# Performance work log

Hardware: AMD Instinct MI355X
Metric: run time of the kernel (lower is better)

The kernel has to match this reference:

```python
import jax, jax.numpy as jnp
import numpy as np

B, S, M, E, H = 4, 2048, 1024, 8, 4096
CAP = 2 * (B * S) // E  # GShard top-2 capacity = 2*s/e = 2048


def setup_inputs() -> dict:
    key = jax.random.key(0)
    k = jax.random.split(key, 6)
    sc = 0.02
    return {
        "x": jax.random.normal(k[0], (B, S, M), jnp.float32),
        "wg": jax.random.normal(k[1], (M, E), jnp.float32) * sc,
        "w1": jax.random.normal(k[2], (E, M, H), jnp.float32) * sc,
        "b1": jnp.zeros((E, H), jnp.float32),
        "w2": jax.random.normal(k[3], (E, H, M), jnp.float32) * sc,
        "b2": jnp.zeros((E, M), jnp.float32),
    }


def top2gating(logits, capacity):
    # Faithful GShard/fairscale top2gating: logits [s, e]
    s, e = logits.shape
    gates = jax.nn.softmax(logits, axis=-1)
    idx1 = jnp.argmax(gates, axis=1)
    mask1 = jax.nn.one_hot(idx1, e, dtype=jnp.float32)
    logits2 = jnp.where(mask1 > 0, -jnp.inf, logits)
    idx2 = jnp.argmax(logits2, axis=1)
    mask2 = jax.nn.one_hot(idx2, e, dtype=jnp.float32)
    # positions within each expert's buffer
    loc1 = jnp.cumsum(mask1, axis=0) - 1.0
    loc2 = jnp.cumsum(mask2, axis=0) - 1.0 + jnp.sum(mask1, axis=0, keepdims=True)
    # load-balancing aux loss (computed before capacity drop, per fairscale)
    me = jnp.mean(gates, axis=0)
    ce = jnp.mean(mask1, axis=0)
    l_aux = jnp.mean(me * ce) * (e * e)
    # drop tokens over capacity
    mask1 = mask1 * (loc1 < capacity)
    mask2 = mask2 * (loc2 < capacity)
    loc1_s = jnp.sum(loc1 * mask1, axis=1).astype(jnp.int32)
    loc2_s = jnp.sum(loc2 * mask2, axis=1).astype(jnp.int32)
    gates1 = jnp.sum(gates * mask1, axis=1)
    gates2 = jnp.sum(gates * mask2, axis=1)
    denom = jnp.maximum(gates1 + gates2, 1e-9)
    gates1 = gates1 / denom
    gates2 = gates2 / denom
    # dense [s, e, c] combine weights (as in the original einsum formulation)
    oh1 = jax.nn.one_hot(loc1_s, capacity, dtype=jnp.float32)
    oh2 = jax.nn.one_hot(loc2_s, capacity, dtype=jnp.float32)
    combine = (gates1[:, None] * mask1)[:, :, None] * oh1[:, None, :] \
            + (gates2[:, None] * mask2)[:, :, None] * oh2[:, None, :]
    dispatch = combine > 0
    return l_aux, combine, dispatch


def reference(x, wg, w1, b1, w2, b2):
    d_model = x.shape[2]
    xf = x.reshape(-1, d_model)                      # [s, m]
    logits = xf @ wg                                 # [s, e]
    l_aux, combine, dispatch = top2gating(logits, CAP)
    # dispatch: dense one-hot scatter, as in torch.einsum('sec,sm->ecm')
    disp = jnp.einsum('sec,sm->ecm', dispatch.astype(xf.dtype), xf)
    # per-expert FFN (Linear -> ReLU -> Linear), vectorized over experts
    h = jax.nn.relu(jnp.einsum('ecm,emh->ech', disp, w1) + b1[:, None, :])
    eo = jnp.einsum('ech,ehm->ecm', h, w2) + b2[:, None, :]
    # combine: torch.einsum('sec,ecm->sm')
    out = jnp.einsum('sec,ecm->sm', combine, eo)
    return out.reshape(x.shape), l_aux
```

## Files before the change

kernel.cpp:

```cpp
#include <hip/hip_runtime.h>
#include <stdint.h>

typedef unsigned short u16;
typedef __attribute__((ext_vector_type(8))) short bf16x8;
typedef __attribute__((ext_vector_type(4))) float f32x4;

#define TOKENS 8192
#define DM 1024
#define NE 8
#define DH 4096
#define CAP 2048

__device__ __forceinline__ u16 f2bf(float f) {
  unsigned int u = __float_as_uint(f);
  u = u + 0x7FFFu + ((u >> 16) & 1u);
  return (u16)(u >> 16);
}

__device__ __forceinline__ void gll16(const void* g, void* l) {
  __builtin_amdgcn_global_load_lds(
      (const __attribute__((address_space(1))) unsigned int*)g,
      (__attribute__((address_space(3))) unsigned int*)l, 16, 0, 0);
}

__global__ __launch_bounds__(256) void gating_kernel(
    const float* __restrict__ x, const float* __restrict__ wg,
    int* __restrict__ idx1, int* __restrict__ idx2,
    float* __restrict__ g1r, float* __restrict__ g2r, float* __restrict__ me) {
  __shared__ float gsh[4][8];
  int lane = threadIdx.x & 63;
  int w = threadIdx.x >> 6;
  int t = blockIdx.x * 4 + w;
  const float* xr = x + (size_t)t * DM;
  double acc[8];
#pragma unroll
  for (int e = 0; e < 8; ++e) acc[e] = 0.0;
#pragma unroll
  for (int it = 0; it < 4; ++it) {
    float4 xv = ((const float4*)xr)[it * 64 + lane];
    int base = (it * 64 + lane) * 4;
    const float* wr = wg + (size_t)base * 8;
    float xs[4] = {xv.x, xv.y, xv.z, xv.w};
#pragma unroll
    for (int j = 0; j < 4; ++j)
#pragma unroll
      for (int e = 0; e < 8; ++e) acc[e] += (double)xs[j] * (double)wr[j * 8 + e];
  }
#pragma unroll
  for (int off = 32; off > 0; off >>= 1)
#pragma unroll
    for (int e = 0; e < 8; ++e) acc[e] += __shfl_down(acc[e], off);
  if (lane == 0) {
    float l[8];
#pragma unroll
    for (int e = 0; e < 8; ++e) l[e] = (float)acc[e];
    int i1 = 0;
    float v1 = l[0];
#pragma unroll
    for (int e = 1; e < 8; ++e)
      if (l[e] > v1) { v1 = l[e]; i1 = e; }
    int i2 = -1;
    float v2 = -3.4e38f;
#pragma unroll
    for (int e = 0; e < 8; ++e)
      if (e != i1 && l[e] > v2) { v2 = l[e]; i2 = e; }
    float s = 0.f;
    float p[8];
#pragma unroll
    for (int e = 0; e < 8; ++e) { p[e] = expf(l[e] - v1); s += p[e]; }
    float inv = 1.f / s;
    idx1[t] = i1;
    idx2[t] = i2;
    g1r[t] = inv;
    g2r[t] = expf(v2 - v1) * inv;
#pragma unroll
    for (int e = 0; e < 8; ++e) gsh[w][e] = p[e] * inv;
  }
  __syncthreads();
  if (threadIdx.x < 8) {
    int e = threadIdx.x;
    atomicAdd(&me[e], gsh[0][e] + gsh[1][e] + gsh[2][e] + gsh[3][e]);
  }
}

__global__ __launch_bounds__(1024) void scan_kernel(
    const int* __restrict__ idx1, const int* __restrict__ idx2,
    const float* __restrict__ g1r, const float* __restrict__ g2r,
    const float* __restrict__ me,
    int* __restrict__ slot1, int* __restrict__ slot2,
    float* __restrict__ g1n, float* __restrict__ g2n,
    int* __restrict__ slot2tok, float* __restrict__ laux) {
  __shared__ u16 c[16][1024];
  __shared__ u16 csum[16][32];
  __shared__ int tot[16];
  int tid = threadIdx.x;
  int i1[8], i2[8];
#pragma unroll
  for (int ctr = 0; ctr < 16; ++ctr) c[ctr][tid] = 0;
#pragma unroll
  for (int j = 0; j < 8; ++j) {
    int t = tid * 8 + j;
    i1[j] = idx1[t];
    i2[j] = idx2[t];
    c[i1[j]][tid]++;
    c[8 + i2[j]][tid]++;
  }
  __syncthreads();
  if (tid < 512) {
    int ctr = tid >> 5, ch = tid & 31;
    int s = 0;
#pragma unroll
    for (int i = 0; i < 32; ++i) s += c[ctr][ch * 32 + i];
    csum[ctr][ch] = (u16)s;
  }
  __syncthreads();
  if (tid < 16) {
    int run = 0;
#pragma unroll
    for (int ch = 0; ch < 32; ++ch) {
      int v = csum[tid][ch];
      csum[tid][ch] = (u16)run;
      run += v;
    }
    tot[tid] = run;
  }
  __syncthreads();
  if (tid < 512) {
    int ctr = tid >> 5, ch = tid & 31;
    int run = csum[ctr][ch];
#pragma unroll
    for (int i = 0; i < 32; ++i) {
      int v = c[ctr][ch * 32 + i];
      c[ctr][ch * 32 + i] = (u16)run;
      run += v;
    }
  }
  __syncthreads();
#pragma unroll
  for (int j = 0; j < 8; ++j) {
    int t = tid * 8 + j;
    int e1 = i1[j], e2 = i2[j];
    int L1 = c[e1][tid]++;
    int L2 = c[8 + e2][tid]++;
    L2 += tot[e2];
    bool kv1 = L1 < CAP, kv2 = L2 < CAP;
    float G1 = kv1 ? g1r[t] : 0.f;
    float G2 = kv2 ? g2r[t] : 0.f;
    float den = fmaxf(G1 + G2, 1e-9f);
    g1n[t] = G1 / den;
    g2n[t] = G2 / den;
    int s1 = kv1 ? (e1 * CAP + L1) : -1;
    int s2 = kv2 ? (e2 * CAP + L2) : -1;
    slot1[t] = s1;
    slot2[t] = s2;
    if (kv1) slot2tok[s1] = t;
    if (kv2) slot2tok[s2] = t;
  }
  if (tid == 0) {
    double a = 0.0;
    for (int e = 0; e < 8; ++e)
      a += ((double)me[e] / 8192.0) * ((double)tot[e] / 8192.0);
    laux[0] = (float)(a * 8.0);
  }
}

__global__ void transpose_kernel(const float* __restrict__ src, u16* __restrict__ dst,
                                 int R, int C) {
  __shared__ float tile[32][33];
  int tx = threadIdx.x, ty = threadIdx.y;
  int r0 = blockIdx.y * 32, c0 = blockIdx.x * 32;
  const float* s = src + (size_t)blockIdx.z * R * C;
  u16* d = dst + (size_t)blockIdx.z * R * C;
#pragma unroll
  for (int i = 0; i < 32; i += 8) tile[ty + i][tx] = s[(size_t)(r0 + ty + i) * C + c0 + tx];
  __syncthreads();
#pragma unroll
  for (int i = 0; i < 32; i += 8)
    d[(size_t)(c0 + ty + i) * R + r0 + tx] = f2bf(tile[tx][ty + i]);
}

__global__ void gather_kernel(const float* __restrict__ x, const int* __restrict__ slot2tok,
                              u16* __restrict__ xe) {
  int slot = blockIdx.y * CAP + blockIdx.x;
  int tok = slot2tok[slot];
  int tid = threadIdx.x;
  u16 o[8];
  if (tok >= 0) {
    const float4* xr = (const float4*)(x + (size_t)tok * DM);
    float4 a = xr[tid * 2], b = xr[tid * 2 + 1];
    o[0] = f2bf(a.x); o[1] = f2bf(a.y); o[2] = f2bf(a.z); o[3] = f2bf(a.w);
    o[4] = f2bf(b.x); o[5] = f2bf(b.y); o[6] = f2bf(b.z); o[7] = f2bf(b.w);
  } else {
#pragma unroll
    for (int j = 0; j < 8; ++j) o[j] = 0;
  }
  *(uint4*)(xe + (size_t)slot * DM + tid * 8) = *(const uint4*)o;
}

#define BAR()                              \
  {                                        \
    asm volatile("" ::: "memory");         \
    __builtin_amdgcn_s_barrier();          \
    asm volatile("" ::: "memory");         \
  }
#define VMCNT(n) asm volatile("s_waitcnt vmcnt(" #n ")" ::: "memory")

template <int RELU, int OUTBF16>
__global__ __launch_bounds__(512, 2) void gemm_kernel(
    const u16* __restrict__ A, const u16* __restrict__ Bt,
    const float* __restrict__ bias, void* __restrict__ Cv,
    int MO, int NO, int K) {
  __shared__ __align__(16) u16 As[2][256 * 64];
  __shared__ __align__(16) u16 Bs[2][256 * 64];
  const int tid = threadIdx.x;
  const int lane = tid & 63, wid = tid >> 6;
  const int wm = wid >> 2, wn = wid & 3;

  const int gx = gridDim.x, gy = gridDim.y;
  const int nwg = gx * gy * gridDim.z;
  const int L = (blockIdx.z * gy + blockIdx.y) * gx + blockIdx.x;
  const int cpx = nwg >> 3;
  const int Ls = (L & 7) * cpx + (L >> 3);
  const int bx = Ls % gx;
  const int tq = Ls / gx;
  const int by = tq % gy;
  const int eb = tq / gy;

  const size_t Ks2 = (size_t)K * 2;
  const char* Ag = (const char*)(A + (size_t)eb * MO * K + (size_t)by * 256 * K);
  const char* Bg = (const char*)(Bt + (size_t)eb * NO * K + (size_t)bx * 256 * K);
  const int rl = tid >> 3;
  const int sb = ((tid & 7) * 16) ^ ((rl & 7) << 4);
  Ag += (size_t)rl * Ks2 + sb;
  Bg += (size_t)rl * Ks2 + sb;
  char* AsB = ((char*)As) + tid * 16;
  char* BsB = ((char*)Bs) + tid * 16;
  const u16* AsE = &As[0][0];
  const u16* BsE = &Bs[0][0];
  const int fr = lane & 15, kg8 = (lane >> 4) * 8;
  const int swz = (fr & 7) << 3;

#define STAGE_A(BUF_, REG_, KT_) \
  gll16(Ag + (size_t)((REG_)*64) * Ks2 + (size_t)(KT_)*128, AsB + (BUF_)*32768 + (REG_)*8192)
#define STAGE_B(BUF_, REG_, KT_) \
  gll16(Bg + (size_t)((REG_)*64) * Ks2 + (size_t)(KT_)*128, BsB + (BUF_)*32768 + (REG_)*8192)
#define LDA(BUF_, M_, K_) \
  (*(const bf16x8*)&AsE[(BUF_)*16384 + (wm * 128 + (M_)*16 + fr) * 64 + (((K_)*32 + kg8) ^ swz)])
#define LDB(BUF_, N_, K_) \
  (*(const bf16x8*)&BsE[(BUF_)*16384 + (wn * 64 + (N_)*16 + fr) * 64 + (((K_)*32 + kg8) ^ swz)])
#define MFMA_Q(MB_, NB_)                                                            \
  _Pragma("unroll") for (int k = 0; k < 2; ++k)                                     \
  _Pragma("unroll") for (int m = 0; m < 4; ++m)                                     \
  _Pragma("unroll") for (int n = 0; n < 2; ++n)                                     \
      acc[(MB_) + m][(NB_) + n] = __builtin_amdgcn_mfma_f32_16x16x32_bf16(          \
          areg[m][k], breg[(NB_) + n][k], acc[(MB_) + m][(NB_) + n], 0, 0, 0)

  f32x4 acc[8][4];
#pragma unroll
  for (int i = 0; i < 8; ++i)
#pragma unroll
    for (int j = 0; j < 4; ++j) acc[i][j] = {0.f, 0.f, 0.f, 0.f};
  bf16x8 areg[4][2], breg[4][2];

  const int NT = K >> 6;
  STAGE_B(0, 0, 0); STAGE_B(0, 1, 0); STAGE_B(0, 2, 0); STAGE_B(0, 3, 0);
  STAGE_A(0, 0, 0); STAGE_A(0, 1, 0); STAGE_A(0, 2, 0); STAGE_A(0, 3, 0);
  {
    const int s1 = (1 < NT) ? 1 : 0;
    STAGE_B(1, 0, s1); STAGE_B(1, 1, s1); STAGE_B(1, 2, s1); STAGE_B(1, 3, s1);
  }
  VMCNT(4);
  BAR();

#define PHASE_SET(CUR_, NXT_, STA_, STB_)                                           \
  {                                                                                 \
                        \
    _Pragma("unroll") for (int m = 0; m < 4; ++m) {                                 \
      areg[m][0] = LDA(CUR_, m, 0); areg[m][1] = LDA(CUR_, m, 1);                   \
    }                                                                               \
    _Pragma("unroll") for (int n = 0; n < 2; ++n) {                                 \
      breg[n][0] = LDB(CUR_, n, 0); breg[n][1] = LDB(CUR_, n, 1);                   \
    }                                                                               \
    STAGE_A(NXT_, 0, STA_); STAGE_A(NXT_, 1, STA_);                                 \
    STAGE_A(NXT_, 2, STA_); STAGE_A(NXT_, 3, STA_);                                 \
    BAR();                                                                          \
    __builtin_amdgcn_s_setprio(1); MFMA_Q(0, 0); __builtin_amdgcn_s_setprio(0);     \
    BAR();                                                                          \
                                                            \
    _Pragma("unroll") for (int n = 2; n < 4; ++n) {                                 \
      breg[n][0] = LDB(CUR_, n, 0); breg[n][1] = LDB(CUR_, n, 1);                   \
    }                                                                               \
    BAR();                                                                          \
    __builtin_amdgcn_s_setprio(1); MFMA_Q(0, 2); __builtin_amdgcn_s_setprio(0);     \
    BAR();                                                                          \
       \
    _Pragma("unroll") for (int m = 0; m < 4; ++m) {                                 \
      areg[m][0] = LDA(CUR_, 4 + m, 0); areg[m][1] = LDA(CUR_, 4 + m, 1);           \
    }                                                                               \
    STAGE_B(CUR_, 0, STB_); STAGE_B(CUR_, 1, STB_);                                 \
    BAR();                                                                          \
    __builtin_amdgcn_s_setprio(1); MFMA_Q(4, 0); __builtin_amdgcn_s_setprio(0);     \
    BAR();                                                                          \
      \
    STAGE_B(CUR_, 2, STB_); STAGE_B(CUR_, 3, STB_);                                 \
    VMCNT(4);                                                                       \
    BAR();                                                                          \
    __builtin_amdgcn_s_setprio(1); MFMA_Q(4, 2); __builtin_amdgcn_s_setprio(0);     \
    BAR();                                                                          \
  }

  for (int t = 0; t < NT; t += 2) {
    const int sa1 = (t + 1 < NT) ? t + 1 : NT - 1;
    const int sb1 = (t + 2 < NT) ? t + 2 : NT - 1;
    const int sa2 = (t + 2 < NT) ? t + 2 : NT - 1;
    const int sb2 = (t + 3 < NT) ? t + 3 : NT - 1;
    PHASE_SET(0, 1, sa1, sb1);
    PHASE_SET(1, 0, sa2, sb2);
  }

  const int row0 = by * 256 + wm * 128 + (kg8 >> 3) * 4;
  const int col0 = bx * 256 + wn * 64 + fr;
  const float* be = bias + (size_t)eb * NO;
  size_t cbase = (size_t)eb * MO * NO;
#pragma unroll
  for (int m = 0; m < 8; ++m) {
#pragma unroll
    for (int n = 0; n < 4; ++n) {
      int col = col0 + n * 16;
      float bv = be[col];
#pragma unroll
      for (int r = 0; r < 4; ++r) {
        int row = row0 + m * 16 + r;
        float v = acc[m][n][r] + bv;
        if (RELU) v = fmaxf(v, 0.f);
        if (OUTBF16)
          ((u16*)Cv)[cbase + (size_t)row * NO + col] = f2bf(v);
        else
          ((float*)Cv)[cbase + (size_t)row * NO + col] = v;
      }
    }
  }
#undef PHASE_SET
#undef STAGE_A
#undef STAGE_B
#undef LDA
#undef LDB
#undef MFMA_Q
}

__global__ void combine_kernel(const float* __restrict__ eo,
                               const float* __restrict__ g1n, const float* __restrict__ g2n,
                               const int* __restrict__ slot1, const int* __restrict__ slot2,
                               float* __restrict__ out) {
  int t = blockIdx.x, tid = threadIdx.x;
  float g1 = g1n[t], g2 = g2n[t];
  int s1 = slot1[t], s2 = slot2[t];
  float4 o = make_float4(0.f, 0.f, 0.f, 0.f);
  if (s1 >= 0) {
    float4 a = ((const float4*)(eo + (size_t)s1 * DM))[tid];
    o.x = g1 * a.x; o.y = g1 * a.y; o.z = g1 * a.z; o.w = g1 * a.w;
  }
  if (s2 >= 0) {
    float4 b = ((const float4*)(eo + (size_t)s2 * DM))[tid];
    o.x += g2 * b.x; o.y += g2 * b.y; o.z += g2 * b.z; o.w += g2 * b.w;
  }
  ((float4*)(out + (size_t)t * DM))[tid] = o;
}

extern "C" void kernel_launch(void* const* d_in, const int* in_sizes, int n_in,
                              void* d_out, int out_size, void* d_ws, size_t ws_size,
                              hipStream_t stream) {
  const float* x = (const float*)d_in[0];
  const float* wg = (const float*)d_in[1];
  const float* w1 = (const float*)d_in[2];
  const float* b1 = (const float*)d_in[3];
  const float* w2 = (const float*)d_in[4];
  const float* b2 = (const float*)d_in[5];
  float* out = (float*)d_out;

  const size_t SZ_WT1 = (size_t)NE * DH * DM * 2;
  const size_t SZ_WT2 = (size_t)NE * DM * DH * 2;
  const size_t SZ_XE = (size_t)NE * CAP * DM * 2;
  const size_t SZ_H = (size_t)NE * CAP * DH * 2;
  const size_t SZ_TOK = (size_t)TOKENS * 4;

  char* p = (char*)d_ws;
  u16* wt1 = (u16*)p;
  float* eo = (float*)p;            p += SZ_WT1;
  u16* wt2 = (u16*)p;               p += SZ_WT2;
  u16* xe = (u16*)p;                p += SZ_XE;
  u16* h = (u16*)p;                 p += SZ_H;
  int* idx1 = (int*)p;              p += SZ_TOK;
  int* idx2 = (int*)p;              p += SZ_TOK;
  int* slot1 = (int*)p;             p += SZ_TOK;
  int* slot2 = (int*)p;             p += SZ_TOK;
  float* g1r = (float*)p;           p += SZ_TOK;
  float* g2r = (float*)p;           p += SZ_TOK;
  float* g1n = (float*)p;           p += SZ_TOK;
  float* g2n = (float*)p;           p += SZ_TOK;
  int* slot2tok = (int*)p;          p += (size_t)NE * CAP * 4;
  float* me = (float*)p;            p += 256;
  if ((size_t)(p - (char*)d_ws) > ws_size) return;

  hipMemsetAsync(me, 0, 32, stream);
  hipMemsetAsync(slot2tok, 0xFF, (size_t)NE * CAP * 4, stream);

  gating_kernel<<<TOKENS / 4, 256, 0, stream>>>(x, wg, idx1, idx2, g1r, g2r, me);
  scan_kernel<<<1, 1024, 0, stream>>>(idx1, idx2, g1r, g2r, me, slot1, slot2, g1n, g2n,
                                      slot2tok, out + (size_t)TOKENS * DM);
  transpose_kernel<<<dim3(DH / 32, DM / 32, NE), dim3(32, 8), 0, stream>>>(w1, wt1, DM, DH);
  transpose_kernel<<<dim3(DM / 32, DH / 32, NE), dim3(32, 8), 0, stream>>>(w2, wt2, DH, DM);
  gather_kernel<<<dim3(CAP, NE), 128, 0, stream>>>(x, slot2tok, xe);
  gemm_kernel<1, 1><<<dim3(DH / 256, CAP / 256, NE), 512, 0, stream>>>(xe, wt1, b1, (void*)h,
                                                                       CAP, DH, DM);
  gemm_kernel<0, 0><<<dim3(DM / 256, CAP / 256, NE), 512, 0, stream>>>(h, wt2, b2, (void*)eo,
                                                                       CAP, DM, DH);
  combine_kernel<<<TOKENS, 256, 0, stream>>>(eo, g1n, g2n, slot1, slot2, out);
}
```

Baseline: 470.9 us.

## Replace fine-grained 8-barrier GEMM pipeline with simple double-buffered tile step

Restructures the GEMM main loop from an interleaved schedule with many barriers per K-tile, where B staging runs ahead of A within the same buffer, into a plain double-buffered loop. Each step issues all A and B global->LDS loads for the next tile, computes the current tile, then waits with vmcnt(0) and one barrier. This removes most barrier overhead but gives up the finer overlap of loads with MFMA and waits for all outstanding loads each step, which may expose memory latency.

```diff
diff --git a/kernel.cpp b/kernel.cpp
--- a/kernel.cpp
+++ b/kernel.cpp
@@ -263,59 +263,45 @@
   bf16x8 areg[4][2], breg[4][2];
 
   const int NT = K >> 6;
-  STAGE_B(0, 0, 0); STAGE_B(0, 1, 0); STAGE_B(0, 2, 0); STAGE_B(0, 3, 0);
-  STAGE_A(0, 0, 0); STAGE_A(0, 1, 0); STAGE_A(0, 2, 0); STAGE_A(0, 3, 0);
-  {
-    const int s1 = (1 < NT) ? 1 : 0;
-    STAGE_B(1, 0, s1); STAGE_B(1, 1, s1); STAGE_B(1, 2, s1); STAGE_B(1, 3, s1);
-  }
-  VMCNT(4);
-  BAR();
-
-#define PHASE_SET(CUR_, NXT_, STA_, STB_)                                           \
+
+#define TILE_STEP(CUR_, NXT_, ST_)                                                  \
   {                                                                                 \
-                        \
+                          \
+    STAGE_A(NXT_, 0, ST_); STAGE_A(NXT_, 1, ST_);                                   \
+    STAGE_A(NXT_, 2, ST_); STAGE_A(NXT_, 3, ST_);                                   \
+    STAGE_B(NXT_, 0, ST_); STAGE_B(NXT_, 1, ST_);                                   \
+    STAGE_B(NXT_, 2, ST_); STAGE_B(NXT_, 3, ST_);                                   \
+                                   \
     _Pragma("unroll") for (int m = 0; m < 4; ++m) {                                 \
       areg[m][0] = LDA(CUR_, m, 0); areg[m][1] = LDA(CUR_, m, 1);                   \
     }                                                                               \
-    _Pragma("unroll") for (int n = 0; n < 2; ++n) {                                 \
+    _Pragma("unroll") for (int n = 0; n < 4; ++n) {                                 \
       breg[n][0] = LDB(CUR_, n, 0); breg[n][1] = LDB(CUR_, n, 1);                   \
     }                                                                               \
-    STAGE_A(NXT_, 0, STA_); STAGE_A(NXT_, 1, STA_);                                 \
-    STAGE_A(NXT_, 2, STA_); STAGE_A(NXT_, 3, STA_);                                 \
-    BAR();                                                                          \
-    __builtin_amdgcn_s_setprio(1); MFMA_Q(0, 0); __builtin_amdgcn_s_setprio(0);     \
-    BAR();                                                                          \
-                                                            \
-    _Pragma("unroll") for (int n = 2; n < 4; ++n) {                                 \
-      breg[n][0] = LDB(CUR_, n, 0); breg[n][1] = LDB(CUR_, n, 1);                   \
-    }                                                                               \
-    BAR();                                                                          \
-    __builtin_amdgcn_s_setprio(1); MFMA_Q(0, 2); __builtin_amdgcn_s_setprio(0);     \
-    BAR();                                                                          \
-       \
+    __builtin_amdgcn_s_setprio(1);                                                  \
+    MFMA_Q(0, 0); MFMA_Q(0, 2);                                                     \
+    __builtin_amdgcn_s_setprio(0);                                                  \
+                          \
     _Pragma("unroll") for (int m = 0; m < 4; ++m) {                                 \
       areg[m][0] = LDA(CUR_, 4 + m, 0); areg[m][1] = LDA(CUR_, 4 + m, 1);           \
     }                                                                               \
-    STAGE_B(CUR_, 0, STB_); STAGE_B(CUR_, 1, STB_);                                 \
-    BAR();                                                                          \
-    __builtin_amdgcn_s_setprio(1); MFMA_Q(4, 0); __builtin_amdgcn_s_setprio(0);     \
-    BAR();                                                                          \
-      \
-    STAGE_B(CUR_, 2, STB_); STAGE_B(CUR_, 3, STB_);                                 \
-    VMCNT(4);                                                                       \
-    BAR();                                                                          \
-    __builtin_amdgcn_s_setprio(1); MFMA_Q(4, 2); __builtin_amdgcn_s_setprio(0);     \
-    BAR();                                                                          \
-  }
+    __builtin_amdgcn_s_setprio(1);                                                  \
+    MFMA_Q(4, 0); MFMA_Q(4, 2);                                                     \
+    __builtin_amdgcn_s_setprio(0);                                                  \
+    VMCNT(0);           \
+    BAR();              \
+  }
+
+  STAGE_A(0, 0, 0); STAGE_A(0, 1, 0); STAGE_A(0, 2, 0); STAGE_A(0, 3, 0);
+  STAGE_B(0, 0, 0); STAGE_B(0, 1, 0); STAGE_B(0, 2, 0); STAGE_B(0, 3, 0);
+  VMCNT(0);
+  BAR();
 
   for (int t = 0; t < NT; t += 2) {
-    const int sa1 = (t + 1 < NT) ? t + 1 : NT - 1;
-    const int sb1 = (t + 2 < NT) ? t + 2 : NT - 1;
-    const int sa2 = (t + 2 < NT) ? t + 2 : NT - 1;
-    const int sb2 = (t + 3 < NT) ? t + 3 : NT - 1;
-    PHASE_SET(0, 1, sa1, sb1);
-    PHASE_SET(1, 0, sa2, sb2);
+    const int s1 = (t + 1 < NT) ? t + 1 : NT - 1;
+    const int s2 = (t + 2 < NT) ? t + 2 : NT - 1;
+    TILE_STEP(0, 1, s1);
+    TILE_STEP(1, 0, s2);
   }
 
   const int row0 = by * 256 + wm * 128 + (kg8 >> 3) * 4;
@@ -340,7 +326,7 @@
       }
     }
   }
-#undef PHASE_SET
+#undef TILE_STEP
 #undef STAGE_A
 #undef STAGE_B
 #undef LDA
```

New measurement: 461.6 us. 1.02x faster.
